# Performance work log

Measured on AMD Instinct MI355X. Metric: run time of the kernel, lower is better.

Reference implementation:

```python
import jax, jax.numpy as jnp
import numpy as np

DIM = 64  # head dim, init arg
SCALE = DIM ** -0.5

def setup_inputs() -> dict:
    key = jax.random.key(0)
    kq, kk, kv = jax.random.split(key, 3)
    shape = (4, 2048, 8, 64)  # (b, n, h, d)
    q = jax.random.normal(kq, shape, dtype=jnp.float32)
    k = jax.random.normal(kk, shape, dtype=jnp.float32)
    v = jax.random.normal(kv, shape, dtype=jnp.float32)
    return {"q": q, "k": k, "v": v}

def reference(q, k, v):
    # score: [b, h, n_q, n_k] -- matches torch bmm over (b*h) batched [n, d] x [d, n]
    score = jnp.einsum('bqhd,bkhd->bhqk', q, k) * SCALE
    attn = jax.nn.softmax(score, axis=-1)
    # context back to [b, n, h, d] (torch permutes h,b,n,d -> b,n,h,d)
    context = jnp.einsum('bhqk,bkhd->bqhd', attn, v)
    return context
```

## Files before the change

### kernel.cpp

```cpp
#include <hip/hip_runtime.h>

#define B 4
#define N 2048
#define H 8
#define D 64
#define HD 512
#define QT 128
#define KT 64
#define NTILES (N / KT)
#define PLS 72

typedef _Float16 half8 __attribute__((ext_vector_type(8)));
typedef float float4_ __attribute__((ext_vector_type(4)));
typedef float float16_ __attribute__((ext_vector_type(16)));

__global__ void prep_kernel(const float* __restrict__ K, const float* __restrict__ V,
                            _Float16* __restrict__ Kf, _Float16* __restrict__ Vtr) {
    __shared__ _Float16 tile[64][PLS];
    const int t = threadIdx.x;
    if (blockIdx.x < 2048) {
        const size_t i = (size_t)blockIdx.x * 256 + t;
        const float4_* p = (const float4_*)(K + i * 8);
        float4_ a = p[0], b = p[1];
        half8 hh;
        #pragma unroll
        for (int j = 0; j < 4; ++j) { hh[j] = (_Float16)a[j]; hh[4 + j] = (_Float16)b[j]; }
        *(half8*)(Kf + i * 8) = hh;
    } else {
        const int bid = blockIdx.x - 2048;
        const int nt = bid & 31, h = (bid >> 5) & 7, b = bid >> 8;
        {
            const int i = t >> 2, c0 = (t & 3) * 16;
            const float* vp = V + (size_t)b * N * HD + (size_t)(nt * 64 + i) * HD + h * D + c0;
            #pragma unroll
            for (int j = 0; j < 4; ++j) {
                float4_ a = *(const float4_*)(vp + j * 4);
                #pragma unroll
                for (int c = 0; c < 4; ++c) tile[i][c0 + j * 4 + c] = (_Float16)a[c];
            }
        }
        __syncthreads();
        {
            const int d = t >> 2, n0 = (t & 3) * 16;
            half8 w0, w1;
            #pragma unroll
            for (int j = 0; j < 4; ++j) {
                w0[j]     = tile[n0 + j][d];
                w0[4 + j] = tile[n0 + 8 + j][d];
                w1[j]     = tile[n0 + 4 + j][d];
                w1[4 + j] = tile[n0 + 12 + j][d];
            }
            _Float16* op = Vtr + ((size_t)(b * H + h) * D + d) * N + nt * 64 + n0;
            *(half8*)op = w0;
            *(half8*)(op + 8) = w1;
        }
    }
}

__device__ __forceinline__ void stage_k(const _Float16* __restrict__ Kbh, int keybase,
                                        _Float16* kb, int wave, int lane) {
    const int rsub = lane >> 3, slot = lane & 7;
    #pragma unroll
    for (int i = 0; i < 2; ++i) {
        const int row = wave * 16 + i * 8 + rsub;
        const int c = slot ^ (row & 7);
        __builtin_amdgcn_global_load_lds(
            (const __attribute__((address_space(1))) void*)(Kbh + (size_t)(keybase + row) * HD + c * 8),
            (__attribute__((address_space(3))) void*)(kb + (wave * 16 + i * 8) * 64), 16, 0, 0);
    }
}
__device__ __forceinline__ void stage_v(const _Float16* __restrict__ Vbh, int keybase,
                                        _Float16* vb, int wave, int lane) {
    const int rsub = lane >> 3, slot = lane & 7;
    #pragma unroll
    for (int i = 0; i < 2; ++i) {
        const int row = wave * 16 + i * 8 + rsub;
        const int c = slot ^ (row & 7);
        __builtin_amdgcn_global_load_lds(
            (const __attribute__((address_space(1))) void*)(Vbh + (size_t)row * N + keybase + c * 8),
            (__attribute__((address_space(3))) void*)(vb + (wave * 16 + i * 8) * 64), 16, 0, 0);
    }
}

static __device__ __forceinline__ void do_s(const _Float16* __restrict__ Kt,
                                            const half8 qf[4], float& lsum,
                                            half8 pf[4], int ln, int hi) {
    float16_ s0 = {}, s1 = {};
    __builtin_amdgcn_s_setprio(1);
    #pragma unroll
    for (int ks = 0; ks < 4; ++ks) {
        const int csw = ((2 * ks + hi) ^ (ln & 7)) * 8;
        half8 a0 = *(const half8*)(Kt + ln * 64 + csw);
        half8 a1 = *(const half8*)(Kt + (32 + ln) * 64 + csw);
        s0 = __builtin_amdgcn_mfma_f32_32x32x16_f16(a0, qf[ks], s0, 0, 0, 0);
        s1 = __builtin_amdgcn_mfma_f32_32x32x16_f16(a1, qf[ks], s1, 0, 0, 0);
    }
    __builtin_amdgcn_s_setprio(0);
    #pragma unroll
    for (int kb = 0; kb < 2; ++kb) {
        const float16_ s = kb ? s1 : s0;
        half8 f0, f1;
        #pragma unroll
        for (int j = 0; j < 8; ++j) {
            float pa = __builtin_amdgcn_exp2f(s[j]);
            float pb = __builtin_amdgcn_exp2f(s[8 + j]);
            lsum += pa + pb;
            f0[j] = (_Float16)pa;
            f1[j] = (_Float16)pb;
        }
        pf[2 * kb]     = f0;
        pf[2 * kb + 1] = f1;
    }
}

static __device__ __forceinline__ void do_pv(const _Float16* __restrict__ Vtile,
                                             const half8 pf[4], float16_& o0, float16_& o1,
                                             int ln, int hi) {
    __builtin_amdgcn_s_setprio(1);
    #pragma unroll
    for (int ks = 0; ks < 4; ++ks) {
        const int csw = ((2 * ks + hi) ^ (ln & 7)) * 8;
        half8 b0 = *(const half8*)(Vtile + ln * 64 + csw);
        half8 b1 = *(const half8*)(Vtile + (32 + ln) * 64 + csw);
        o0 = __builtin_amdgcn_mfma_f32_32x32x16_f16(pf[ks], b0, o0, 0, 0, 0);
        o1 = __builtin_amdgcn_mfma_f32_32x32x16_f16(pf[ks], b1, o1, 0, 0, 0);
    }
    __builtin_amdgcn_s_setprio(0);
}

__global__ __launch_bounds__(256, 2)
void fattn7_kernel(const float* __restrict__ Q, const _Float16* __restrict__ Kf,
                   const _Float16* __restrict__ Vt, float* __restrict__ Out)
{
    __shared__ __align__(16) _Float16 Kb[2][KT * 64];
    __shared__ __align__(16) _Float16 Vb[2][D * 64];

    const int tid  = threadIdx.x;
    const int wave = tid >> 6;
    const int lane = tid & 63;
    const int ln   = lane & 31;
    const int hi   = lane >> 5;

    const int h = blockIdx.y;
    const int b = blockIdx.z;
    const int q_base = blockIdx.x * QT + wave * 32;

    const size_t bh_q = (size_t)b * N * HD + (size_t)h * D;
    const _Float16* Kbh = Kf + bh_q;
    const _Float16* Vbh = Vt + (size_t)(b * H + h) * D * N;

    const float SC = 0.125f * 1.4426950408889634f;
    half8 qf[4];
    {
        const float* qp = Q + bh_q + (size_t)(q_base + ln) * HD + hi * 8;
        #pragma unroll
        for (int ks = 0; ks < 4; ++ks) {
            float4_ a0 = *(const float4_*)(qp + ks * 16);
            float4_ a1 = *(const float4_*)(qp + ks * 16 + 4);
            half8 f;
            #pragma unroll
            for (int j = 0; j < 4; ++j) { f[j] = (_Float16)(a0[j] * SC); f[4 + j] = (_Float16)(a1[j] * SC); }
            qf[ks] = f;
        }
    }

    float16_ o0 = {}, o1 = {};
    float lsum = 0.f;
    half8 pf[4];

    stage_k(Kbh, 0, Kb[0], wave, lane);
    __syncthreads();
    stage_k(Kbh, KT, Kb[1], wave, lane);
    stage_v(Vbh, 0, Vb[0], wave, lane);
    do_s(Kb[0], qf, lsum, pf, ln, hi);

    for (int t = 1; t < NTILES; ++t) {
        __syncthreads();
        if (t + 1 < NTILES)
            stage_k(Kbh, (t + 1) * KT, Kb[(t + 1) & 1], wave, lane);
        stage_v(Vbh, t * KT, Vb[t & 1], wave, lane);

        do_pv(Vb[(t - 1) & 1], pf, o0, o1, ln, hi);
        do_s(Kb[t & 1], qf, lsum, pf, ln, hi);
    }

    __syncthreads();
    do_pv(Vb[(NTILES - 1) & 1], pf, o0, o1, ln, hi);

    lsum += __shfl_xor(lsum, 32, 64);
    const float inv = 1.0f / lsum;
    #pragma unroll
    for (int r = 0; r < 16; ++r) {
        const int rl = (r & 3) + 8 * (r >> 2) + 4 * hi;
        const float linv = __shfl(inv, rl, 64);
        const size_t ro = bh_q + (size_t)(q_base + rl) * HD;
        Out[ro + ln]      = o0[r] * linv;
        Out[ro + 32 + ln] = o1[r] * linv;
    }
}

__global__ __launch_bounds__(256, 2)
void fattn_fb_kernel(const float* __restrict__ Q, const float* __restrict__ K,
                     const float* __restrict__ V, float* __restrict__ Out)
{
    __shared__ __align__(16) _Float16 Ks[KT][PLS];
    __shared__ __align__(16) _Float16 Vts[D][PLS];
    __shared__ __align__(16) _Float16 Pwf[4][16][PLS];
    const int tid = threadIdx.x, wave = tid >> 6, lane = tid & 63;
    const int m = lane & 15, quad = lane >> 4;
    const int q_base = blockIdx.x * 64;
    const size_t bh_off = ((size_t)blockIdx.z * N * H + (size_t)blockIdx.y) * D;
    const float SCALE = 0.125f;
    const int qrow = q_base + wave * 16 + m;
    const float* qp = Q + bh_off + (size_t)qrow * HD + quad * 8;
    half8 qf0, qf1;
    #pragma unroll
    for (int j = 0; j < 8; ++j) qf0[j] = (_Float16)(qp[j] * SCALE);
    #pragma unroll
    for (int j = 0; j < 8; ++j) qf1[j] = (_Float16)(qp[32 + j] * SCALE);
    float4_ o[4] = {};
    float mi[4], li[4];
    #pragma unroll
    for (int r = 0; r < 4; ++r) { mi[r] = -1e30f; li[r] = 0.0f; }
    for (int kt = 0; kt < N; kt += KT) {
        __syncthreads();
        {
            const int key = tid >> 2, c0 = (tid & 3) * 16;
            const float* kp = K + bh_off + (size_t)(kt + key) * HD + c0;
            half8 lo, hi;
            #pragma unroll
            for (int j = 0; j < 8; ++j) lo[j] = (_Float16)kp[j];
            #pragma unroll
            for (int j = 0; j < 8; ++j) hi[j] = (_Float16)kp[8 + j];
            *(half8*)&Ks[key][c0] = lo;
            *(half8*)&Ks[key][c0 + 8] = hi;
        }
        {
            const int c0 = (tid & 15) * 4, k0 = (tid >> 4) * 4;
            const float* vp = V + bh_off + (size_t)(kt + k0) * HD + c0;
            #pragma unroll
            for (int c = 0; c < 4; ++c)
                #pragma unroll
                for (int i = 0; i < 4; ++i)
                    Vts[c0 + c][k0 + i] = (_Float16)vp[i * HD + c];
        }
        __syncthreads();
        float4_ s[4];
        #pragma unroll
        for (int blk = 0; blk < 4; ++blk) {
            const int key = blk * 16 + m;
            half8 kf0 = *(const half8*)&Ks[key][quad * 8];
            half8 kf1 = *(const half8*)&Ks[key][32 + quad * 8];
            float4_ acc = {};
            acc = __builtin_amdgcn_mfma_f32_16x16x32_f16(qf0, kf0, acc, 0, 0, 0);
            acc = __builtin_amdgcn_mfma_f32_16x16x32_f16(qf1, kf1, acc, 0, 0, 0);
            s[blk] = acc;
        }
        float alpha[4];
        #pragma unroll
        for (int r = 0; r < 4; ++r) {
            float v0 = fmaxf(fmaxf(s[0][r], s[1][r]), fmaxf(s[2][r], s[3][r]));
            #pragma unroll
            for (int mask = 1; mask < 16; mask <<= 1) v0 = fmaxf(v0, __shfl_xor(v0, mask, 64));
            float mn = fmaxf(mi[r], v0);
            alpha[r] = __expf(mi[r] - mn);
            mi[r] = mn;
        }
        #pragma unroll
        for (int blk = 0; blk < 4; ++blk)
            #pragma unroll
            for (int r = 0; r < 4; ++r) s[blk][r] = __expf(s[blk][r] - mi[r]);
        #pragma unroll
        for (int r = 0; r < 4; ++r) {
            float tt = s[0][r] + s[1][r] + s[2][r] + s[3][r];
            #pragma unroll
            for (int mask = 1; mask < 16; mask <<= 1) tt += __shfl_xor(tt, mask, 64);
            li[r] = li[r] * alpha[r] + tt;
        }
        #pragma unroll
        for (int d = 0; d < 4; ++d)
            #pragma unroll
            for (int r = 0; r < 4; ++r) o[d][r] *= alpha[r];
        #pragma unroll
        for (int blk = 0; blk < 4; ++blk)
            #pragma unroll
            for (int r = 0; r < 4; ++r)
                Pwf[wave][quad * 4 + r][blk * 16 + m] = (_Float16)s[blk][r];
        #pragma unroll
        for (int ks = 0; ks < 2; ++ks) {
            half8 af = *(const half8*)&Pwf[wave][m][ks * 32 + quad * 8];
            #pragma unroll
            for (int d = 0; d < 4; ++d) {
                half8 bf = *(const half8*)&Vts[d * 16 + m][ks * 32 + quad * 8];
                o[d] = __builtin_amdgcn_mfma_f32_16x16x32_f16(af, bf, o[d], 0, 0, 0);
            }
        }
    }
    #pragma unroll
    for (int d = 0; d < 4; ++d)
        #pragma unroll
        for (int r = 0; r < 4; ++r) {
            const int row = q_base + wave * 16 + quad * 4 + r;
            Out[bh_off + (size_t)row * HD + d * 16 + m] = o[d][r] / li[r];
        }
}

extern "C" void kernel_launch(void* const* d_in, const int* in_sizes, int n_in,
                              void* d_out, int out_size, void* d_ws, size_t ws_size,
                              hipStream_t stream) {
    const float* q = (const float*)d_in[0];
    const float* k = (const float*)d_in[1];
    const float* v = (const float*)d_in[2];
    float* out = (float*)d_out;

    const size_t nelem = (size_t)B * N * H * D;
    const size_t need = 2 * nelem * sizeof(_Float16);

    if (ws_size >= need) {
        _Float16* Kf = (_Float16*)d_ws;
        _Float16* Vtr = Kf + nelem;
        prep_kernel<<<dim3(2048 + 1024), 256, 0, stream>>>(k, v, Kf, Vtr);
        fattn7_kernel<<<dim3(N / QT, H, B), 256, 0, stream>>>(q, Kf, Vtr, out);
    } else {
        fattn_fb_kernel<<<dim3(N / 64, H, B), 256, 0, stream>>>(q, k, v, out);
    }
}
```

Measured before the change: 136.4 us.

## Double per-wave query rows and triple-buffer K/V staging with explicit vmcnt waits

Each wave now handles 64 query rows, two 32-row blocks, instead of 32, so every K/V fragment read from LDS feeds twice as many MFMAs. The K and V tiles move to a three-buffer ring prefetched two tiles ahead, and the block syncs with s_waitcnt vmcnt plus s_barrier rather than __syncthreads. The S and PV stages are no longer software-pipelined across tiles. The grid shrinks to 256 blocks with launch bounds of one block per CU, which raises register pressure and cuts occupancy and parallelism on a large-CU GPU.

```diff
diff --git a/kernel.cpp b/kernel.cpp
--- a/kernel.cpp
+++ b/kernel.cpp
@@ -5,7 +5,7 @@
 #define H 8
 #define D 64
 #define HD 512
-#define QT 128
+#define QT 256
 #define KT 64
 #define NTILES (N / KT)
 #define PLS 72
@@ -13,6 +13,8 @@
 typedef _Float16 half8 __attribute__((ext_vector_type(8)));
 typedef float float4_ __attribute__((ext_vector_type(4)));
 typedef float float16_ __attribute__((ext_vector_type(16)));
+
+#define MFMA32(a, b, c) __builtin_amdgcn_mfma_f32_32x32x16_f16((a), (b), (c), 0, 0, 0)
 
 __global__ void prep_kernel(const float* __restrict__ K, const float* __restrict__ V,
                             _Float16* __restrict__ Kf, _Float16* __restrict__ Vtr) {
@@ -82,58 +84,12 @@
     }
 }
 
-static __device__ __forceinline__ void do_s(const _Float16* __restrict__ Kt,
-                                            const half8 qf[4], float& lsum,
-                                            half8 pf[4], int ln, int hi) {
-    float16_ s0 = {}, s1 = {};
-    __builtin_amdgcn_s_setprio(1);
-    #pragma unroll
-    for (int ks = 0; ks < 4; ++ks) {
-        const int csw = ((2 * ks + hi) ^ (ln & 7)) * 8;
-        half8 a0 = *(const half8*)(Kt + ln * 64 + csw);
-        half8 a1 = *(const half8*)(Kt + (32 + ln) * 64 + csw);
-        s0 = __builtin_amdgcn_mfma_f32_32x32x16_f16(a0, qf[ks], s0, 0, 0, 0);
-        s1 = __builtin_amdgcn_mfma_f32_32x32x16_f16(a1, qf[ks], s1, 0, 0, 0);
-    }
-    __builtin_amdgcn_s_setprio(0);
-    #pragma unroll
-    for (int kb = 0; kb < 2; ++kb) {
-        const float16_ s = kb ? s1 : s0;
-        half8 f0, f1;
-        #pragma unroll
-        for (int j = 0; j < 8; ++j) {
-            float pa = __builtin_amdgcn_exp2f(s[j]);
-            float pb = __builtin_amdgcn_exp2f(s[8 + j]);
-            lsum += pa + pb;
-            f0[j] = (_Float16)pa;
-            f1[j] = (_Float16)pb;
-        }
-        pf[2 * kb]     = f0;
-        pf[2 * kb + 1] = f1;
-    }
-}
-
-static __device__ __forceinline__ void do_pv(const _Float16* __restrict__ Vtile,
-                                             const half8 pf[4], float16_& o0, float16_& o1,
-                                             int ln, int hi) {
-    __builtin_amdgcn_s_setprio(1);
-    #pragma unroll
-    for (int ks = 0; ks < 4; ++ks) {
-        const int csw = ((2 * ks + hi) ^ (ln & 7)) * 8;
-        half8 b0 = *(const half8*)(Vtile + ln * 64 + csw);
-        half8 b1 = *(const half8*)(Vtile + (32 + ln) * 64 + csw);
-        o0 = __builtin_amdgcn_mfma_f32_32x32x16_f16(pf[ks], b0, o0, 0, 0, 0);
-        o1 = __builtin_amdgcn_mfma_f32_32x32x16_f16(pf[ks], b1, o1, 0, 0, 0);
-    }
-    __builtin_amdgcn_s_setprio(0);
-}
-
-__global__ __launch_bounds__(256, 2)
-void fattn7_kernel(const float* __restrict__ Q, const _Float16* __restrict__ Kf,
+__global__ __launch_bounds__(256, 1)
+void fattn8_kernel(const float* __restrict__ Q, const _Float16* __restrict__ Kf,
                    const _Float16* __restrict__ Vt, float* __restrict__ Out)
 {
-    __shared__ __align__(16) _Float16 Kb[2][KT * 64];
-    __shared__ __align__(16) _Float16 Vb[2][D * 64];
+    __shared__ __align__(16) _Float16 KbA[KT * 64], KbB[KT * 64], KbC[KT * 64];
+    __shared__ __align__(16) _Float16 VbA[D * 64],  VbB[D * 64],  VbC[D * 64];
 
     const int tid  = threadIdx.x;
     const int wave = tid >> 6;
@@ -143,16 +99,17 @@
 
     const int h = blockIdx.y;
     const int b = blockIdx.z;
-    const int q_base = blockIdx.x * QT + wave * 32;
+    const int q_base = blockIdx.x * QT + wave * 64;
 
     const size_t bh_q = (size_t)b * N * HD + (size_t)h * D;
     const _Float16* Kbh = Kf + bh_q;
     const _Float16* Vbh = Vt + (size_t)(b * H + h) * D * N;
 
     const float SC = 0.125f * 1.4426950408889634f;
-    half8 qf[4];
-    {
-        const float* qp = Q + bh_q + (size_t)(q_base + ln) * HD + hi * 8;
+    half8 qf[2][4];
+    #pragma unroll
+    for (int qb = 0; qb < 2; ++qb) {
+        const float* qp = Q + bh_q + (size_t)(q_base + qb * 32 + ln) * HD + hi * 8;
         #pragma unroll
         for (int ks = 0; ks < 4; ++ks) {
             float4_ a0 = *(const float4_*)(qp + ks * 16);
@@ -160,42 +117,88 @@
             half8 f;
             #pragma unroll
             for (int j = 0; j < 4; ++j) { f[j] = (_Float16)(a0[j] * SC); f[4 + j] = (_Float16)(a1[j] * SC); }
-            qf[ks] = f;
-        }
-    }
-
-    float16_ o0 = {}, o1 = {};
-    float lsum = 0.f;
-    half8 pf[4];
-
-    stage_k(Kbh, 0, Kb[0], wave, lane);
-    __syncthreads();
-    stage_k(Kbh, KT, Kb[1], wave, lane);
-    stage_v(Vbh, 0, Vb[0], wave, lane);
-    do_s(Kb[0], qf, lsum, pf, ln, hi);
-
-    for (int t = 1; t < NTILES; ++t) {
-        __syncthreads();
-        if (t + 1 < NTILES)
-            stage_k(Kbh, (t + 1) * KT, Kb[(t + 1) & 1], wave, lane);
-        stage_v(Vbh, t * KT, Vb[t & 1], wave, lane);
-
-        do_pv(Vb[(t - 1) & 1], pf, o0, o1, ln, hi);
-        do_s(Kb[t & 1], qf, lsum, pf, ln, hi);
-    }
-
-    __syncthreads();
-    do_pv(Vb[(NTILES - 1) & 1], pf, o0, o1, ln, hi);
-
-    lsum += __shfl_xor(lsum, 32, 64);
-    const float inv = 1.0f / lsum;
-    #pragma unroll
-    for (int r = 0; r < 16; ++r) {
-        const int rl = (r & 3) + 8 * (r >> 2) + 4 * hi;
-        const float linv = __shfl(inv, rl, 64);
-        const size_t ro = bh_q + (size_t)(q_base + rl) * HD;
-        Out[ro + ln]      = o0[r] * linv;
-        Out[ro + 32 + ln] = o1[r] * linv;
+            qf[qb][ks] = f;
+        }
+    }
+
+    float16_ o[2][2] = {};
+    float lsum[2] = {0.f, 0.f};
+
+    _Float16 *kc = KbA, *kn = KbB, *kf = KbC;
+    _Float16 *vc = VbA, *vn = VbB, *vf = VbC;
+    stage_k(Kbh, 0, kc, wave, lane);  stage_v(Vbh, 0, vc, wave, lane);
+    stage_k(Kbh, KT, kn, wave, lane); stage_v(Vbh, KT, vn, wave, lane);
+
+    for (int t = 0; t < NTILES; ++t) {
+        if (t < NTILES - 1) asm volatile("s_waitcnt vmcnt(4)" ::: "memory");
+        else                asm volatile("s_waitcnt vmcnt(0)" ::: "memory");
+        __builtin_amdgcn_s_barrier();
+        __builtin_amdgcn_sched_barrier(0);
+        if (t + 2 < NTILES) {
+            stage_k(Kbh, (t + 2) * KT, kf, wave, lane);
+            stage_v(Vbh, (t + 2) * KT, vf, wave, lane);
+        }
+
+        half8 pf[2][4];
+        #pragma unroll
+        for (int kb = 0; kb < 2; ++kb) {
+            float16_ s0 = {}, s1 = {};
+            __builtin_amdgcn_s_setprio(1);
+            #pragma unroll
+            for (int ks = 0; ks < 4; ++ks) {
+                const int csw = ((2 * ks + hi) ^ (ln & 7)) * 8;
+                half8 a = *(const half8*)(kc + (kb * 32 + ln) * 64 + csw);
+                s0 = MFMA32(a, qf[0][ks], s0);
+                s1 = MFMA32(a, qf[1][ks], s1);
+            }
+            __builtin_amdgcn_s_setprio(0);
+            #pragma unroll
+            for (int qb = 0; qb < 2; ++qb) {
+                const float16_ s = qb ? s1 : s0;
+                half8 f0, f1;
+                #pragma unroll
+                for (int j = 0; j < 8; ++j) {
+                    float pa = __builtin_amdgcn_exp2f(s[j]);
+                    float pb = __builtin_amdgcn_exp2f(s[8 + j]);
+                    lsum[qb] += pa + pb;
+                    f0[j] = (_Float16)pa;
+                    f1[j] = (_Float16)pb;
+                }
+                pf[qb][2 * kb]     = f0;
+                pf[qb][2 * kb + 1] = f1;
+            }
+        }
+
+        __builtin_amdgcn_s_setprio(1);
+        #pragma unroll
+        for (int ks = 0; ks < 4; ++ks) {
+            const int csw = ((2 * ks + hi) ^ (ln & 7)) * 8;
+            half8 b0 = *(const half8*)(vc + ln * 64 + csw);
+            half8 b1 = *(const half8*)(vc + (32 + ln) * 64 + csw);
+            o[0][0] = MFMA32(pf[0][ks], b0, o[0][0]);
+            o[0][1] = MFMA32(pf[0][ks], b1, o[0][1]);
+            o[1][0] = MFMA32(pf[1][ks], b0, o[1][0]);
+            o[1][1] = MFMA32(pf[1][ks], b1, o[1][1]);
+        }
+        __builtin_amdgcn_s_setprio(0);
+
+        _Float16* tk = kc; kc = kn; kn = kf; kf = tk;
+        _Float16* tv = vc; vc = vn; vn = vf; vf = tv;
+    }
+
+    #pragma unroll
+    for (int qb = 0; qb < 2; ++qb) {
+        float v = lsum[qb];
+        v += __shfl_xor(v, 32, 64);
+        const float inv = 1.0f / v;
+        #pragma unroll
+        for (int r = 0; r < 16; ++r) {
+            const int rl = (r & 3) + 8 * (r >> 2) + 4 * hi;
+            const float linv = __shfl(inv, rl, 64);
+            const size_t ro = bh_q + (size_t)(q_base + qb * 32 + rl) * HD;
+            Out[ro + ln]      = o[qb][0][r] * linv;
+            Out[ro + 32 + ln] = o[qb][1][r] * linv;
+        }
     }
 }
 
@@ -320,7 +323,7 @@
         _Float16* Kf = (_Float16*)d_ws;
         _Float16* Vtr = Kf + nelem;
         prep_kernel<<<dim3(2048 + 1024), 256, 0, stream>>>(k, v, Kf, Vtr);
-        fattn7_kernel<<<dim3(N / QT, H, B), 256, 0, stream>>>(q, Kf, Vtr, out);
+        fattn8_kernel<<<dim3(N / QT, H, B), 256, 0, stream>>>(q, Kf, Vtr, out);
     } else {
         fattn_fb_kernel<<<dim3(N / 64, H, B), 256, 0, stream>>>(q, k, v, out);
     }
```

Result: slower. 143.5 us (+5.2%).

## Split key range across two wave groups per block with LDS reduction

Applied to the files above, without the earlier changes.

The attention kernel now runs 512 threads per block, where two groups of four waves each process half of the key sequence with their own double-buffered K/V LDS staging. At the end, partial outputs and row sums from the second group are reduced through shared memory before normalization and store. The software pipeline is also reworked to prefetch two tiles ahead using explicit vmcnt waits and raw barriers instead of overlapping PV of the previous tile with S of the current one. This doubles waves per query tile to improve latency hiding and occupancy, at the cost of 64KB LDS per block and an extra reduction step.

```diff
diff --git a/kernel.cpp b/kernel.cpp
--- a/kernel.cpp
+++ b/kernel.cpp
@@ -7,12 +7,14 @@
 #define HD 512
 #define QT 128
 #define KT 64
-#define NTILES (N / KT)
+#define NT2 16
 #define PLS 72
 
 typedef _Float16 half8 __attribute__((ext_vector_type(8)));
 typedef float float4_ __attribute__((ext_vector_type(4)));
 typedef float float16_ __attribute__((ext_vector_type(16)));
+
+#define MFMA32(a, b, c) __builtin_amdgcn_mfma_f32_32x32x16_f16((a), (b), (c), 0, 0, 0)
 
 __global__ void prep_kernel(const float* __restrict__ K, const float* __restrict__ V,
                             _Float16* __restrict__ Kf, _Float16* __restrict__ Vtr) {
@@ -58,96 +60,54 @@
 }
 
 __device__ __forceinline__ void stage_k(const _Float16* __restrict__ Kbh, int keybase,
-                                        _Float16* kb, int wave, int lane) {
+                                        _Float16* kb, int wg, int lane) {
     const int rsub = lane >> 3, slot = lane & 7;
     #pragma unroll
     for (int i = 0; i < 2; ++i) {
-        const int row = wave * 16 + i * 8 + rsub;
+        const int row = wg * 16 + i * 8 + rsub;
         const int c = slot ^ (row & 7);
         __builtin_amdgcn_global_load_lds(
             (const __attribute__((address_space(1))) void*)(Kbh + (size_t)(keybase + row) * HD + c * 8),
-            (__attribute__((address_space(3))) void*)(kb + (wave * 16 + i * 8) * 64), 16, 0, 0);
+            (__attribute__((address_space(3))) void*)(kb + (wg * 16 + i * 8) * 64), 16, 0, 0);
     }
 }
 __device__ __forceinline__ void stage_v(const _Float16* __restrict__ Vbh, int keybase,
-                                        _Float16* vb, int wave, int lane) {
+                                        _Float16* vb, int wg, int lane) {
     const int rsub = lane >> 3, slot = lane & 7;
     #pragma unroll
     for (int i = 0; i < 2; ++i) {
-        const int row = wave * 16 + i * 8 + rsub;
+        const int row = wg * 16 + i * 8 + rsub;
         const int c = slot ^ (row & 7);
         __builtin_amdgcn_global_load_lds(
             (const __attribute__((address_space(1))) void*)(Vbh + (size_t)row * N + keybase + c * 8),
-            (__attribute__((address_space(3))) void*)(vb + (wave * 16 + i * 8) * 64), 16, 0, 0);
-    }
-}
-
-static __device__ __forceinline__ void do_s(const _Float16* __restrict__ Kt,
-                                            const half8 qf[4], float& lsum,
-                                            half8 pf[4], int ln, int hi) {
-    float16_ s0 = {}, s1 = {};
-    __builtin_amdgcn_s_setprio(1);
-    #pragma unroll
-    for (int ks = 0; ks < 4; ++ks) {
-        const int csw = ((2 * ks + hi) ^ (ln & 7)) * 8;
-        half8 a0 = *(const half8*)(Kt + ln * 64 + csw);
-        half8 a1 = *(const half8*)(Kt + (32 + ln) * 64 + csw);
-        s0 = __builtin_amdgcn_mfma_f32_32x32x16_f16(a0, qf[ks], s0, 0, 0, 0);
-        s1 = __builtin_amdgcn_mfma_f32_32x32x16_f16(a1, qf[ks], s1, 0, 0, 0);
-    }
-    __builtin_amdgcn_s_setprio(0);
-    #pragma unroll
-    for (int kb = 0; kb < 2; ++kb) {
-        const float16_ s = kb ? s1 : s0;
-        half8 f0, f1;
-        #pragma unroll
-        for (int j = 0; j < 8; ++j) {
-            float pa = __builtin_amdgcn_exp2f(s[j]);
-            float pb = __builtin_amdgcn_exp2f(s[8 + j]);
-            lsum += pa + pb;
-            f0[j] = (_Float16)pa;
-            f1[j] = (_Float16)pb;
-        }
-        pf[2 * kb]     = f0;
-        pf[2 * kb + 1] = f1;
-    }
-}
-
-static __device__ __forceinline__ void do_pv(const _Float16* __restrict__ Vtile,
-                                             const half8 pf[4], float16_& o0, float16_& o1,
-                                             int ln, int hi) {
-    __builtin_amdgcn_s_setprio(1);
-    #pragma unroll
-    for (int ks = 0; ks < 4; ++ks) {
-        const int csw = ((2 * ks + hi) ^ (ln & 7)) * 8;
-        half8 b0 = *(const half8*)(Vtile + ln * 64 + csw);
-        half8 b1 = *(const half8*)(Vtile + (32 + ln) * 64 + csw);
-        o0 = __builtin_amdgcn_mfma_f32_32x32x16_f16(pf[ks], b0, o0, 0, 0, 0);
-        o1 = __builtin_amdgcn_mfma_f32_32x32x16_f16(pf[ks], b1, o1, 0, 0, 0);
-    }
-    __builtin_amdgcn_s_setprio(0);
-}
-
-__global__ __launch_bounds__(256, 2)
-void fattn7_kernel(const float* __restrict__ Q, const _Float16* __restrict__ Kf,
-                   const _Float16* __restrict__ Vt, float* __restrict__ Out)
+            (__attribute__((address_space(3))) void*)(vb + (wg * 16 + i * 8) * 64), 16, 0, 0);
+    }
+}
+
+__global__ __launch_bounds__(512, 4)
+void fattn10_kernel(const float* __restrict__ Q, const _Float16* __restrict__ Kf,
+                    const _Float16* __restrict__ Vt, float* __restrict__ Out)
 {
-    __shared__ __align__(16) _Float16 Kb[2][KT * 64];
-    __shared__ __align__(16) _Float16 Vb[2][D * 64];
+    static __shared__ __align__(16) _Float16 smem[32768];
 
     const int tid  = threadIdx.x;
     const int wave = tid >> 6;
     const int lane = tid & 63;
     const int ln   = lane & 31;
     const int hi   = lane >> 5;
+    const int qg   = wave & 3;
+    const int kh   = wave >> 2;
 
     const int h = blockIdx.y;
     const int b = blockIdx.z;
-    const int q_base = blockIdx.x * QT + wave * 32;
+    const int q_base = blockIdx.x * QT + qg * 32;
 
     const size_t bh_q = (size_t)b * N * HD + (size_t)h * D;
     const _Float16* Kbh = Kf + bh_q;
     const _Float16* Vbh = Vt + (size_t)(b * H + h) * D * N;
+
+    _Float16* Kbuf = smem + kh * 8192;
+    _Float16* Vbuf = smem + 16384 + kh * 8192;
 
     const float SC = 0.125f * 1.4426950408889634f;
     half8 qf[4];
@@ -166,36 +126,94 @@
 
     float16_ o0 = {}, o1 = {};
     float lsum = 0.f;
-    half8 pf[4];
-
-    stage_k(Kbh, 0, Kb[0], wave, lane);
+
+    const int tbase = kh * NT2 * KT;
+    stage_k(Kbh, tbase, Kbuf, qg, lane);              stage_v(Vbh, tbase, Vbuf, qg, lane);
+    stage_k(Kbh, tbase + KT, Kbuf + 4096, qg, lane);  stage_v(Vbh, tbase + KT, Vbuf + 4096, qg, lane);
+
+    for (int t = 0; t < NT2; ++t) {
+        if (t < NT2 - 1) asm volatile("s_waitcnt vmcnt(4)" ::: "memory");
+        else             asm volatile("s_waitcnt vmcnt(0)" ::: "memory");
+        __builtin_amdgcn_s_barrier();
+        __builtin_amdgcn_sched_barrier(0);
+
+        const _Float16* kc = Kbuf + (t & 1) * 4096;
+        const _Float16* vc = Vbuf + (t & 1) * 4096;
+
+        half8 pf[4];
+        #pragma unroll
+        for (int kb = 0; kb < 2; ++kb) {
+            float16_ s = {};
+            __builtin_amdgcn_s_setprio(1);
+            #pragma unroll
+            for (int ks = 0; ks < 4; ++ks) {
+                const int csw = ((2 * ks + hi) ^ (ln & 7)) * 8;
+                half8 a = *(const half8*)(kc + (kb * 32 + ln) * 64 + csw);
+                s = MFMA32(a, qf[ks], s);
+            }
+            __builtin_amdgcn_s_setprio(0);
+            half8 f0, f1;
+            #pragma unroll
+            for (int j = 0; j < 8; ++j) {
+                float pa = __builtin_amdgcn_exp2f(s[j]);
+                float pb = __builtin_amdgcn_exp2f(s[8 + j]);
+                lsum += pa + pb;
+                f0[j] = (_Float16)pa;
+                f1[j] = (_Float16)pb;
+            }
+            pf[2 * kb]     = f0;
+            pf[2 * kb + 1] = f1;
+        }
+
+        __builtin_amdgcn_s_setprio(1);
+        #pragma unroll
+        for (int ks = 0; ks < 4; ++ks) {
+            const int csw = ((2 * ks + hi) ^ (ln & 7)) * 8;
+            half8 b0 = *(const half8*)(vc + ln * 64 + csw);
+            half8 b1 = *(const half8*)(vc + (32 + ln) * 64 + csw);
+            o0 = MFMA32(pf[ks], b0, o0);
+            o1 = MFMA32(pf[ks], b1, o1);
+        }
+        __builtin_amdgcn_s_setprio(0);
+
+        if (t + 2 < NT2) {
+            __builtin_amdgcn_s_barrier();
+            __builtin_amdgcn_sched_barrier(0);
+            stage_k(Kbh, tbase + (t + 2) * KT, Kbuf + (t & 1) * 4096, qg, lane);
+            stage_v(Vbh, tbase + (t + 2) * KT, Vbuf + (t & 1) * 4096, qg, lane);
+        }
+    }
+
     __syncthreads();
-    stage_k(Kbh, KT, Kb[1], wave, lane);
-    stage_v(Vbh, 0, Vb[0], wave, lane);
-    do_s(Kb[0], qf, lsum, pf, ln, hi);
-
-    for (int t = 1; t < NTILES; ++t) {
-        __syncthreads();
-        if (t + 1 < NTILES)
-            stage_k(Kbh, (t + 1) * KT, Kb[(t + 1) & 1], wave, lane);
-        stage_v(Vbh, t * KT, Vb[t & 1], wave, lane);
-
-        do_pv(Vb[(t - 1) & 1], pf, o0, o1, ln, hi);
-        do_s(Kb[t & 1], qf, lsum, pf, ln, hi);
-    }
-
+    float* cb = (float*)smem;
+    float* ls = cb + 4 * 2 * 16 * 64;
+    if (kh == 1) {
+        #pragma unroll
+        for (int r = 0; r < 16; ++r) {
+            cb[((qg * 2 + 0) * 16 + r) * 64 + lane] = o0[r];
+            cb[((qg * 2 + 1) * 16 + r) * 64 + lane] = o1[r];
+        }
+        ls[qg * 64 + lane] = lsum;
+    }
     __syncthreads();
-    do_pv(Vb[(NTILES - 1) & 1], pf, o0, o1, ln, hi);
-
-    lsum += __shfl_xor(lsum, 32, 64);
-    const float inv = 1.0f / lsum;
-    #pragma unroll
-    for (int r = 0; r < 16; ++r) {
-        const int rl = (r & 3) + 8 * (r >> 2) + 4 * hi;
-        const float linv = __shfl(inv, rl, 64);
-        const size_t ro = bh_q + (size_t)(q_base + rl) * HD;
-        Out[ro + ln]      = o0[r] * linv;
-        Out[ro + 32 + ln] = o1[r] * linv;
+    if (kh == 0) {
+        #pragma unroll
+        for (int r = 0; r < 16; ++r) {
+            o0[r] += cb[((qg * 2 + 0) * 16 + r) * 64 + lane];
+            o1[r] += cb[((qg * 2 + 1) * 16 + r) * 64 + lane];
+        }
+        lsum += ls[qg * 64 + lane];
+        float v = lsum;
+        v += __shfl_xor(v, 32, 64);
+        const float inv = 1.0f / v;
+        #pragma unroll
+        for (int r = 0; r < 16; ++r) {
+            const int rl = (r & 3) + 8 * (r >> 2) + 4 * hi;
+            const float linv = __shfl(inv, rl, 64);
+            const size_t ro = bh_q + (size_t)(q_base + rl) * HD;
+            Out[ro + ln]      = o0[r] * linv;
+            Out[ro + 32 + ln] = o1[r] * linv;
+        }
     }
 }
 
@@ -320,7 +338,7 @@
         _Float16* Kf = (_Float16*)d_ws;
         _Float16* Vtr = Kf + nelem;
         prep_kernel<<<dim3(2048 + 1024), 256, 0, stream>>>(k, v, Kf, Vtr);
-        fattn7_kernel<<<dim3(N / QT, H, B), 256, 0, stream>>>(q, Kf, Vtr, out);
+        fattn10_kernel<<<dim3(N / QT, H, B), 512, 0, stream>>>(q, Kf, Vtr, out);
     } else {
         fattn_fb_kernel<<<dim3(N / 64, H, B), 256, 0, stream>>>(q, k, v, out);
     }
```

Result: no change. 134.3 us (-1.6%).
